# Performance work log

Measured on AMD Instinct MI355X. Metric: run time of the kernel, lower is better.

The kernel has to match this reference:

```python
import jax, jax.numpy as jnp
import numpy as np

N_NODES = 100000


def setup_inputs() -> dict:
    key = jax.random.key(0)
    ks = jax.random.split(key, 6)
    x = jax.random.normal(ks[0], (N_NODES, 3), dtype=jnp.float32)
    edge_index = jax.random.randint(ks[1], (2, 1600000), 0, N_NODES, dtype=jnp.int32)
    W1 = jax.random.normal(ks[2], (6, 64), dtype=jnp.float32) * 0.2
    b1 = jnp.zeros((64,), dtype=jnp.float32)
    W2 = jax.random.normal(ks[3], (67, 128), dtype=jnp.float32) * 0.1
    b2 = jnp.zeros((128,), dtype=jnp.float32)
    Wc = jax.random.normal(ks[4], (128, 5), dtype=jnp.float32) * 0.1
    bc = jnp.zeros((5,), dtype=jnp.float32)
    return {"x": x, "edge_index": edge_index, "W1": W1, "b1": b1,
            "W2": W2, "b2": b2, "Wc": Wc, "bc": bc}


def _pointnet_conv(h, rel, src, dst, W, b, n):
    # gather neighbor features, MLP on [h_j, pos_j - pos_i], max-aggregate per node
    msg = jnp.concatenate([h[src], rel], axis=-1) @ W + b  # [E, out]
    agg = jax.ops.segment_max(msg, dst, num_segments=n)    # [N, out]
    return jax.nn.relu(agg)  # relu also maps -inf (isolated nodes) to 0


def reference(x, edge_index, W1, b1, W2, b2, Wc, bc):
    src, dst = edge_index[0], edge_index[1]
    pos = x  # forward uses data.x for both x and pos
    rel = pos[src] - pos[dst]                       # [E, 3]
    h = _pointnet_conv(x, rel, src, dst, W1, b1, N_NODES)   # [N, 64]
    h = _pointnet_conv(h, rel, src, dst, W2, b2, N_NODES)   # [N, 128]
    logits = h @ Wc + bc                            # [N, 5]
    return jax.nn.log_softmax(logits, axis=-1)
```

## Files before the change

kernel.cpp:

```cpp
#include <hip/hip_runtime.h>
#include <cstdint>

#define CAP 56
#define NBITS 8
#define BINSZ 256
#define BIN_CAP 5120
#define TILE_E 8192
#define SCANN 512

typedef _Float16 h2 __attribute__((ext_vector_type(2)));
typedef _Float16 h4 __attribute__((ext_vector_type(4)));
typedef _Float16 h8 __attribute__((ext_vector_type(8)));

static __device__ inline h8 pkmax8(h8 a, h8 b) {
#if __has_builtin(__builtin_elementwise_max)
    return __builtin_elementwise_max(a, b);
#else
    h8 r;
    #pragma unroll
    for (int i = 0; i < 8; i += 2) {
        h2 aa = { a[i], a[i+1] }, bb = { b[i], b[i+1] }, rr;
        asm("v_pk_max_f16 %0, %1, %2" : "=v"(rr) : "v"(aa), "v"(bb));
        r[i] = rr.x; r[i+1] = rr.y;
    }
    return r;
#endif
}

__global__ __launch_bounds__(256) void bin_kernel(
    const int* __restrict__ ei, int* __restrict__ bin_cnt,
    int* __restrict__ pairs, int E, int nbins)
{
    __shared__ int hist[SCANN];
    __shared__ int sc[SCANN];
    __shared__ int gbase[SCANN];
    __shared__ int lofs[SCANN];
    __shared__ int words[TILE_E];
    __shared__ unsigned short binOf[TILE_E];
    int t = threadIdx.x;
    for (int i = t; i < SCANN; i += 256) { hist[i] = 0; lofs[i] = 0; }
    __syncthreads();
    int e0 = blockIdx.x * TILE_E;
    int s[32], d[32];
    #pragma unroll
    for (int i = 0; i < 32; ++i) {
        int e = e0 + t + i * 256;
        bool ok = e < E;
        s[i] = ok ? ei[e] : 0;
        d[i] = ok ? ei[E + e] : -1;
        if (ok) atomicAdd(&hist[d[i] >> NBITS], 1);
    }
    __syncthreads();
    sc[t] = hist[t]; sc[t + 256] = hist[t + 256];
    __syncthreads();
    for (int off = 1; off < SCANN; off <<= 1) {
        int i0 = t, i1 = t + 256;
        int v0 = (i0 >= off) ? sc[i0 - off] : 0;
        int v1 = (i1 >= off) ? sc[i1 - off] : 0;
        __syncthreads();
        sc[i0] += v0; sc[i1] += v1;
        __syncthreads();
    }
    for (int i = t; i < nbins; i += 256)
        gbase[i] = atomicAdd(&bin_cnt[i], hist[i]);
    __syncthreads();
    #pragma unroll
    for (int i = 0; i < 32; ++i) {
        if (d[i] >= 0) {
            int b = d[i] >> NBITS;
            int p = atomicAdd(&lofs[b], 1);
            int slot = (sc[b] - hist[b]) + p;
            words[slot] = s[i] | ((d[i] & (BINSZ - 1)) << 17);
            binOf[slot] = (unsigned short)b;
        }
    }
    __syncthreads();
    int total = sc[nbins - 1];
    for (int i = t; i < total; i += 256) {
        int b = binOf[i];
        int off = gbase[b] + (i - (sc[b] - hist[b]));
        if (off < BIN_CAP) pairs[b * BIN_CAP + off] = words[i];
    }
}

__global__ __launch_bounds__(256) void scatter2_kernel(
    const int* __restrict__ pairs, const int* __restrict__ bin_cnt,
    int2* __restrict__ meta, int* __restrict__ bucket,
    int* __restrict__ gtot, int N)
{
    __shared__ int cur[BINSZ];
    __shared__ int lbuck[BINSZ * CAP];
    __shared__ int sc2[BINSZ];
    __shared__ int sbase;
    int t = threadIdx.x;
    int b = blockIdx.x;
    for (int i = t; i < BINSZ; i += 256) cur[i] = 0;
    __syncthreads();
    int cnt = min(bin_cnt[b], BIN_CAP);
    const int* pp = pairs + b * BIN_CAP;
    for (int i = t; i < cnt; i += 256) {
        int w = pp[i];
        int p = atomicAdd(&cur[w >> 17], 1);
        if (p < CAP) lbuck[(w >> 17) * CAP + p] = w & 0x1FFFF;
    }
    __syncthreads();
    int c  = min(cur[t], CAP);
    int pc = (c + 7) & ~7;
    {
        int s0 = (c > 0) ? lbuck[t * CAP] : 0;
        for (int p = c; p < pc; ++p) lbuck[t * CAP + p] = s0;
        sc2[t] = pc;
    }
    __syncthreads();
    for (int off = 1; off < BINSZ; off <<= 1) {
        int v = (t >= off) ? sc2[t - off] : 0;
        __syncthreads();
        sc2[t] += v;
        __syncthreads();
    }
    if (t == BINSZ - 1) sbase = atomicAdd(gtot, sc2[BINSZ - 1]);
    __syncthreads();
    int start = sbase + sc2[t] - pc;
    int n = b * BINSZ + t;
    if (n < N) meta[n] = make_int2(start, c);
    int4* dst = (int4*)bucket;
    const int4* srcv = (const int4*)(lbuck + t * CAP);
    for (int p = 0; p < (pc >> 2); ++p) dst[(start >> 2) + p] = srcv[p];
}

__global__ __launch_bounds__(256) void xpack_kernel(
    const float* __restrict__ x, float4* __restrict__ xp,
    int* __restrict__ bin_cnt, int* __restrict__ gtot, int N)
{
    int n = blockIdx.x * 256 + threadIdx.x;
    if (n < N) xp[n] = make_float4(x[n*3], x[n*3+1], x[n*3+2], 0.f);
    if (blockIdx.x == 0) {
        bin_cnt[threadIdx.x] = 0;
        bin_cnt[threadIdx.x + 256] = 0;
        if (threadIdx.x == 0) *gtot = 0;
    }
}

__global__ __launch_bounds__(256) void agg1_gemm_kernel(
    const float4* __restrict__ xp, const int2* __restrict__ meta,
    const int* __restrict__ bucket, const float* __restrict__ W1,
    const float* __restrict__ b1, const float* __restrict__ W2,
    const float* __restrict__ b2, h4* __restrict__ u2h, int N)
{
    __shared__ float h1s[64 * 72];
    int tid = threadIdx.x;
    int n0  = blockIdx.x * 64;
    int sub = tid & 15;
    int ng  = tid >> 4;

    float4 q0 = ((const float4*)(W1 + 0*64))[sub];
    float4 q1 = ((const float4*)(W1 + 1*64))[sub];
    float4 q2 = ((const float4*)(W1 + 2*64))[sub];
    float4 t0 = ((const float4*)(W1 + 3*64))[sub];
    float4 t1 = ((const float4*)(W1 + 4*64))[sub];
    float4 t2 = ((const float4*)(W1 + 5*64))[sub];
    float4 c0 = make_float4(q0.x+t0.x, q0.y+t0.y, q0.z+t0.z, q0.w+t0.w);
    float4 c1 = make_float4(q1.x+t1.x, q1.y+t1.y, q1.z+t1.z, q1.w+t1.w);
    float4 c2 = make_float4(q2.x+t2.x, q2.y+t2.y, q2.z+t2.z, q2.w+t2.w);
    float4 bb = ((const float4*)b1)[sub];

    #pragma unroll
    for (int pass = 0; pass < 4; ++pass) {
        int nl = pass * 16 + ng;
        int n  = n0 + nl;
        float4 m = make_float4(-3e38f, -3e38f, -3e38f, -3e38f);
        int cnt = 0;
        if (n < N) {
            int2 mt = meta[n];
            cnt = mt.y;
            int rounds = (cnt + 7) & ~7;
            const int4* brow4 = (const int4*)(bucket + mt.x);
            int4 ia = brow4[0], ib = brow4[1];
            for (int j0 = 0; j0 < rounds; j0 += 8) {
                int4 na = brow4[(j0 >> 2) + 2];
                int4 nb = brow4[(j0 >> 2) + 3];
                float4 xs[8];
                xs[0] = xp[ia.x]; xs[1] = xp[ia.y]; xs[2] = xp[ia.z]; xs[3] = xp[ia.w];
                xs[4] = xp[ib.x]; xs[5] = xp[ib.y]; xs[6] = xp[ib.z]; xs[7] = xp[ib.w];
                #pragma unroll
                for (int u = 0; u < 8; ++u) {
                    float4 v;
                    v.x = fmaf(xs[u].x, c0.x, fmaf(xs[u].y, c1.x, xs[u].z * c2.x));
                    v.y = fmaf(xs[u].x, c0.y, fmaf(xs[u].y, c1.y, xs[u].z * c2.y));
                    v.z = fmaf(xs[u].x, c0.z, fmaf(xs[u].y, c1.z, xs[u].z * c2.z));
                    v.w = fmaf(xs[u].x, c0.w, fmaf(xs[u].y, c1.w, xs[u].z * c2.w));
                    m.x = fmaxf(m.x, v.x); m.y = fmaxf(m.y, v.y);
                    m.z = fmaxf(m.z, v.z); m.w = fmaxf(m.w, v.w);
                }
                ia = na; ib = nb;
            }
        }
        float4 xd = (n < N) ? xp[n] : make_float4(0.f, 0.f, 0.f, 0.f);
        int colphys = ((((nl >> 2) + sub) & 15) << 2) | (nl & 3);
        h1s[(4*sub+0)*72 + colphys] = (cnt > 0) ? fmaxf(m.x + bb.x - (xd.x*t0.x + xd.y*t1.x + xd.z*t2.x), 0.f) : 0.f;
        h1s[(4*sub+1)*72 + colphys] = (cnt > 0) ? fmaxf(m.y + bb.y - (xd.x*t0.y + xd.y*t1.y + xd.z*t2.y), 0.f) : 0.f;
        h1s[(4*sub+2)*72 + colphys] = (cnt > 0) ? fmaxf(m.z + bb.z - (xd.x*t0.z + xd.y*t1.z + xd.z*t2.z), 0.f) : 0.f;
        h1s[(4*sub+3)*72 + colphys] = (cnt > 0) ? fmaxf(m.w + bb.w - (xd.x*t0.w + xd.y*t1.w + xd.z*t2.w), 0.f) : 0.f;
    }
    __syncthreads();

    int fi = tid & 31;
    int ni = tid >> 5;
    float acc[8][4];
    #pragma unroll
    for (int r = 0; r < 8; ++r)
        #pragma unroll
        for (int c = 0; c < 4; ++c) acc[r][c] = 0.f;

    const float4* W2v = (const float4*)W2;
    #pragma unroll 4
    for (int k = 0; k < 64; ++k) {
        float4 w  = W2v[k*32 + fi];
        int cga = ((2*ni)     + (k >> 2)) & 15;
        int cgb = ((2*ni + 1) + (k >> 2)) & 15;
        float4 a0 = *(const float4*)&h1s[k*72 + cga*4];
        float4 a1 = *(const float4*)&h1s[k*72 + cgb*4];
        float hv[8] = {a0.x,a0.y,a0.z,a0.w,a1.x,a1.y,a1.z,a1.w};
        #pragma unroll
        for (int r = 0; r < 8; ++r) {
            acc[r][0] = fmaf(hv[r], w.x, acc[r][0]);
            acc[r][1] = fmaf(hv[r], w.y, acc[r][1]);
            acc[r][2] = fmaf(hv[r], w.z, acc[r][2]);
            acc[r][3] = fmaf(hv[r], w.w, acc[r][3]);
        }
    }
    float4 bb2 = ((const float4*)b2)[fi];
    float4 wa = W2v[64*32 + fi], wb = W2v[65*32 + fi], wc = W2v[66*32 + fi];
    #pragma unroll
    for (int r = 0; r < 8; ++r) {
        int n = n0 + ni*8 + r;
        if (n >= N) break;
        float4 xd = xp[n];
        h4 o4;
        o4.x = (_Float16)(acc[r][0] + bb2.x + xd.x*wa.x + xd.y*wb.x + xd.z*wc.x);
        o4.y = (_Float16)(acc[r][1] + bb2.y + xd.x*wa.y + xd.y*wb.y + xd.z*wc.y);
        o4.z = (_Float16)(acc[r][2] + bb2.z + xd.x*wa.z + xd.y*wb.z + xd.z*wc.z);
        o4.w = (_Float16)(acc[r][3] + bb2.w + xd.x*wa.w + xd.y*wb.w + xd.z*wc.w);
        u2h[(size_t)n * 32 + fi] = o4;
    }
}

__global__ __launch_bounds__(256) void agg2_head_kernel(
    const float* __restrict__ x, const int2* __restrict__ meta,
    const int* __restrict__ bucket, const float* __restrict__ W2,
    const h8* __restrict__ u2v, const float* __restrict__ Wc,
    const float* __restrict__ bc, float* __restrict__ out, int N)
{
    int gid = blockIdx.x * 256 + threadIdx.x;
    int n   = gid >> 4;
    int sub = threadIdx.x & 15;
    if (n >= N) return;
    int2 mt = meta[n];
    int cnt = mt.y;
    int rounds = (cnt + 7) & ~7;
    const int4* brow4 = (const int4*)(bucket + mt.x);
    const _Float16 NEG = (_Float16)(-60000.0f);
    h8 hm = { NEG, NEG, NEG, NEG, NEG, NEG, NEG, NEG };
    int4 ia = brow4[0], ib = brow4[1];
    for (int j0 = 0; j0 < rounds; j0 += 8) {
        int4 na = brow4[(j0 >> 2) + 2];
        int4 nb = brow4[(j0 >> 2) + 3];
        h8 v0 = u2v[(size_t)ia.x * 16 + sub];
        h8 v1 = u2v[(size_t)ia.y * 16 + sub];
        h8 v2 = u2v[(size_t)ia.z * 16 + sub];
        h8 v3 = u2v[(size_t)ia.w * 16 + sub];
        h8 v4 = u2v[(size_t)ib.x * 16 + sub];
        h8 v5 = u2v[(size_t)ib.y * 16 + sub];
        h8 v6 = u2v[(size_t)ib.z * 16 + sub];
        h8 v7 = u2v[(size_t)ib.w * 16 + sub];
        hm = pkmax8(hm, v0); hm = pkmax8(hm, v1);
        hm = pkmax8(hm, v2); hm = pkmax8(hm, v3);
        hm = pkmax8(hm, v4); hm = pkmax8(hm, v5);
        hm = pkmax8(hm, v6); hm = pkmax8(hm, v7);
        ia = na; ib = nb;
    }
    const float4* W2v = (const float4*)W2;
    float4 wa0 = W2v[64*32 + sub*2], wa1 = W2v[64*32 + sub*2 + 1];
    float4 wb0 = W2v[65*32 + sub*2], wb1 = W2v[65*32 + sub*2 + 1];
    float4 wc0 = W2v[66*32 + sub*2], wc1 = W2v[66*32 + sub*2 + 1];
    float x0 = x[n*3], x1 = x[n*3+1], x2 = x[n*3+2];
    float hh[8];
    hh[0] = (cnt > 0) ? fmaxf((float)hm[0] - (x0*wa0.x + x1*wb0.x + x2*wc0.x), 0.f) : 0.f;
    hh[1] = (cnt > 0) ? fmaxf((float)hm[1] - (x0*wa0.y + x1*wb0.y + x2*wc0.y), 0.f) : 0.f;
    hh[2] = (cnt > 0) ? fmaxf((float)hm[2] - (x0*wa0.z + x1*wb0.z + x2*wc0.z), 0.f) : 0.f;
    hh[3] = (cnt > 0) ? fmaxf((float)hm[3] - (x0*wa0.w + x1*wb0.w + x2*wc0.w), 0.f) : 0.f;
    hh[4] = (cnt > 0) ? fmaxf((float)hm[4] - (x0*wa1.x + x1*wb1.x + x2*wc1.x), 0.f) : 0.f;
    hh[5] = (cnt > 0) ? fmaxf((float)hm[5] - (x0*wa1.y + x1*wb1.y + x2*wc1.y), 0.f) : 0.f;
    hh[6] = (cnt > 0) ? fmaxf((float)hm[6] - (x0*wa1.z + x1*wb1.z + x2*wc1.z), 0.f) : 0.f;
    hh[7] = (cnt > 0) ? fmaxf((float)hm[7] - (x0*wa1.w + x1*wb1.w + x2*wc1.w), 0.f) : 0.f;

    int g = sub * 8;
    float l0 = 0.f, l1 = 0.f, l2 = 0.f, l3 = 0.f, l4 = 0.f;
    #pragma unroll
    for (int k = 0; k < 8; ++k) {
        l0 = fmaf(hh[k], Wc[(g+k)*5+0], l0);
        l1 = fmaf(hh[k], Wc[(g+k)*5+1], l1);
        l2 = fmaf(hh[k], Wc[(g+k)*5+2], l2);
        l3 = fmaf(hh[k], Wc[(g+k)*5+3], l3);
        l4 = fmaf(hh[k], Wc[(g+k)*5+4], l4);
    }
    #pragma unroll
    for (int off = 8; off > 0; off >>= 1) {
        l0 += __shfl_xor(l0, off);
        l1 += __shfl_xor(l1, off);
        l2 += __shfl_xor(l2, off);
        l3 += __shfl_xor(l3, off);
        l4 += __shfl_xor(l4, off);
    }
    l0 += bc[0]; l1 += bc[1]; l2 += bc[2]; l3 += bc[3]; l4 += bc[4];
    float mx  = fmaxf(fmaxf(fmaxf(l0, l1), fmaxf(l2, l3)), l4);
    float s   = expf(l0-mx) + expf(l1-mx) + expf(l2-mx) + expf(l3-mx) + expf(l4-mx);
    float lse = mx + logf(s);
    if (sub < 5) {
        float v = (sub == 0) ? l0 : (sub == 1) ? l1 : (sub == 2) ? l2
                : (sub == 3) ? l3 : l4;
        out[n*5 + sub] = v - lse;
    }
}

extern "C" void kernel_launch(void* const* d_in, const int* in_sizes, int n_in,
                              void* d_out, int out_size, void* d_ws, size_t ws_size,
                              hipStream_t stream)
{
    const float* x  = (const float*)d_in[0];
    const int*   ei = (const int*)d_in[1];
    const float* W1 = (const float*)d_in[2];
    const float* b1 = (const float*)d_in[3];
    const float* W2 = (const float*)d_in[4];
    const float* b2 = (const float*)d_in[5];
    const float* Wc = (const float*)d_in[6];
    const float* bc = (const float*)d_in[7];
    float* out = (float*)d_out;

    int N = in_sizes[0] / 3;
    int E = in_sizes[1] / 2;
    int nbins = (N + BINSZ - 1) / BINSZ;

    char* ws = (char*)d_ws;
    h4*     u2h     = (h4*)    (ws);
    float4* xp      = (float4*)(ws + 25600000);
    int*    pairs   = (int*)   (ws + 27200000);
    int*    bucket  = (int*)   (ws + 35250000);
    int2*   meta    = (int2*)  (ws + 45000000);
    int*    bin_cnt = (int*)   (ws + 45900000);
    int*    gtot    = (int*)   (ws + 45904096);

    xpack_kernel<<<(N + 255) / 256, 256, 0, stream>>>(x, xp, bin_cnt, gtot, N);
    bin_kernel<<<(E + TILE_E - 1) / TILE_E, 256, 0, stream>>>(
        ei, bin_cnt, pairs, E, nbins);
    scatter2_kernel<<<nbins, 256, 0, stream>>>(pairs, bin_cnt, meta, bucket, gtot, N);

    agg1_gemm_kernel<<<(N + 63) / 64, 256, 0, stream>>>(
        xp, meta, bucket, W1, b1, W2, b2, u2h, N);
    agg2_head_kernel<<<(N * 16 + 255) / 256, 256, 0, stream>>>(
        x, meta, bucket, W2, (const h8*)u2h, Wc, bc, out, N);
}
```

Before: 228.9 us.

## Interleave four node gathers per thread and stage W2 in shared memory

Result: slower. 234.1 us (+2.3%).

```diff
diff --git a/kernel.cpp b/kernel.cpp
--- a/kernel.cpp
+++ b/kernel.cpp
@@ -148,10 +148,17 @@
     const float* __restrict__ b2, h4* __restrict__ u2h, int N)
 {
     __shared__ float h1s[64 * 72];
+    __shared__ float4 W2s[64 * 33];
     int tid = threadIdx.x;
     int n0  = blockIdx.x * 64;
     int sub = tid & 15;
     int ng  = tid >> 4;
+
+    {
+        const float4* W2g = (const float4*)W2;
+        for (int i = tid; i < 64 * 32; i += 256)
+            W2s[(i >> 5) * 33 + (i & 31)] = W2g[i];
+    }
 
     float4 q0 = ((const float4*)(W1 + 0*64))[sub];
     float4 q1 = ((const float4*)(W1 + 1*64))[sub];
@@ -164,43 +171,58 @@
     float4 c2 = make_float4(q2.x+t2.x, q2.y+t2.y, q2.z+t2.z, q2.w+t2.w);
     float4 bb = ((const float4*)b1)[sub];
 
-    #pragma unroll
-    for (int pass = 0; pass < 4; ++pass) {
-        int nl = pass * 16 + ng;
-        int n  = n0 + nl;
-        float4 m = make_float4(-3e38f, -3e38f, -3e38f, -3e38f);
-        int cnt = 0;
-        if (n < N) {
-            int2 mt = meta[n];
-            cnt = mt.y;
-            int rounds = (cnt + 7) & ~7;
-            const int4* brow4 = (const int4*)(bucket + mt.x);
-            int4 ia = brow4[0], ib = brow4[1];
-            for (int j0 = 0; j0 < rounds; j0 += 8) {
-                int4 na = brow4[(j0 >> 2) + 2];
-                int4 nb = brow4[(j0 >> 2) + 3];
-                float4 xs[8];
-                xs[0] = xp[ia.x]; xs[1] = xp[ia.y]; xs[2] = xp[ia.z]; xs[3] = xp[ia.w];
-                xs[4] = xp[ib.x]; xs[5] = xp[ib.y]; xs[6] = xp[ib.z]; xs[7] = xp[ib.w];
-                #pragma unroll
-                for (int u = 0; u < 8; ++u) {
-                    float4 v;
-                    v.x = fmaf(xs[u].x, c0.x, fmaf(xs[u].y, c1.x, xs[u].z * c2.x));
-                    v.y = fmaf(xs[u].x, c0.y, fmaf(xs[u].y, c1.y, xs[u].z * c2.y));
-                    v.z = fmaf(xs[u].x, c0.z, fmaf(xs[u].y, c1.z, xs[u].z * c2.z));
-                    v.w = fmaf(xs[u].x, c0.w, fmaf(xs[u].y, c1.w, xs[u].z * c2.w));
-                    m.x = fmaxf(m.x, v.x); m.y = fmaxf(m.y, v.y);
-                    m.z = fmaxf(m.z, v.z); m.w = fmaxf(m.w, v.w);
-                }
-                ia = na; ib = nb;
+    float4 mm[4];
+    int cnt[4], pcm[4], pcv[4];
+    const int4* br[4];
+    #pragma unroll
+    for (int i = 0; i < 4; ++i) {
+        int n = n0 + i*16 + ng;
+        int2 mt = (n < N) ? meta[n] : make_int2(0, 0);
+        cnt[i] = mt.y;
+        int pc = (mt.y + 7) & ~7;
+        pcv[i] = pc;
+        pcm[i] = (pc > 4) ? pc - 4 : 0;
+        br[i]  = (const int4*)(bucket + (mt.y > 0 ? mt.x : 0));
+        mm[i]  = make_float4(-3e38f, -3e38f, -3e38f, -3e38f);
+    }
+    int maxpc = max(max(pcv[0], pcv[1]), max(pcv[2], pcv[3]));
+    for (int j0 = 0; j0 < maxpc; j0 += 4) {
+        int4 id[4];
+        #pragma unroll
+        for (int i = 0; i < 4; ++i)
+            id[i] = br[i][min(j0, pcm[i]) >> 2];
+        float4 xs[16];
+        #pragma unroll
+        for (int i = 0; i < 4; ++i) {
+            xs[i*4+0] = xp[id[i].x]; xs[i*4+1] = xp[id[i].y];
+            xs[i*4+2] = xp[id[i].z]; xs[i*4+3] = xp[id[i].w];
+        }
+        #pragma unroll
+        for (int i = 0; i < 4; ++i) {
+            #pragma unroll
+            for (int u = 0; u < 4; ++u) {
+                float4 xv = xs[i*4+u];
+                float4 v;
+                v.x = fmaf(xv.x, c0.x, fmaf(xv.y, c1.x, xv.z * c2.x));
+                v.y = fmaf(xv.x, c0.y, fmaf(xv.y, c1.y, xv.z * c2.y));
+                v.z = fmaf(xv.x, c0.z, fmaf(xv.y, c1.z, xv.z * c2.z));
+                v.w = fmaf(xv.x, c0.w, fmaf(xv.y, c1.w, xv.z * c2.w));
+                mm[i].x = fmaxf(mm[i].x, v.x); mm[i].y = fmaxf(mm[i].y, v.y);
+                mm[i].z = fmaxf(mm[i].z, v.z); mm[i].w = fmaxf(mm[i].w, v.w);
             }
         }
+    }
+    #pragma unroll
+    for (int i = 0; i < 4; ++i) {
+        int nl = i*16 + ng;
+        int n  = n0 + nl;
         float4 xd = (n < N) ? xp[n] : make_float4(0.f, 0.f, 0.f, 0.f);
         int colphys = ((((nl >> 2) + sub) & 15) << 2) | (nl & 3);
-        h1s[(4*sub+0)*72 + colphys] = (cnt > 0) ? fmaxf(m.x + bb.x - (xd.x*t0.x + xd.y*t1.x + xd.z*t2.x), 0.f) : 0.f;
-        h1s[(4*sub+1)*72 + colphys] = (cnt > 0) ? fmaxf(m.y + bb.y - (xd.x*t0.y + xd.y*t1.y + xd.z*t2.y), 0.f) : 0.f;
-        h1s[(4*sub+2)*72 + colphys] = (cnt > 0) ? fmaxf(m.z + bb.z - (xd.x*t0.z + xd.y*t1.z + xd.z*t2.z), 0.f) : 0.f;
-        h1s[(4*sub+3)*72 + colphys] = (cnt > 0) ? fmaxf(m.w + bb.w - (xd.x*t0.w + xd.y*t1.w + xd.z*t2.w), 0.f) : 0.f;
+        bool ok = cnt[i] > 0;
+        h1s[(4*sub+0)*72 + colphys] = ok ? fmaxf(mm[i].x + bb.x - (xd.x*t0.x + xd.y*t1.x + xd.z*t2.x), 0.f) : 0.f;
+        h1s[(4*sub+1)*72 + colphys] = ok ? fmaxf(mm[i].y + bb.y - (xd.x*t0.y + xd.y*t1.y + xd.z*t2.y), 0.f) : 0.f;
+        h1s[(4*sub+2)*72 + colphys] = ok ? fmaxf(mm[i].z + bb.z - (xd.x*t0.z + xd.y*t1.z + xd.z*t2.z), 0.f) : 0.f;
+        h1s[(4*sub+3)*72 + colphys] = ok ? fmaxf(mm[i].w + bb.w - (xd.x*t0.w + xd.y*t1.w + xd.z*t2.w), 0.f) : 0.f;
     }
     __syncthreads();
 
@@ -212,10 +234,9 @@
         #pragma unroll
         for (int c = 0; c < 4; ++c) acc[r][c] = 0.f;
 
-    const float4* W2v = (const float4*)W2;
     #pragma unroll 4
     for (int k = 0; k < 64; ++k) {
-        float4 w  = W2v[k*32 + fi];
+        float4 w  = W2s[k*33 + fi];
         int cga = ((2*ni)     + (k >> 2)) & 15;
         int cgb = ((2*ni + 1) + (k >> 2)) & 15;
         float4 a0 = *(const float4*)&h1s[k*72 + cga*4];
@@ -229,6 +250,7 @@
             acc[r][3] = fmaf(hv[r], w.w, acc[r][3]);
         }
     }
+    const float4* W2v = (const float4*)W2;
     float4 bb2 = ((const float4*)b2)[fi];
     float4 wa = W2v[64*32 + fi], wb = W2v[65*32 + fi], wc = W2v[66*32 + fi];
     #pragma unroll
```
